# Kernel tuning notes

Hardware: AMD Instinct MI355X
Metric: run time of the kernel (lower is better)

The kernel has to match this reference:

```python
import jax, jax.numpy as jnp
import numpy as np

B, D, L, H, E = 65536, 3, 64, 256, 8
N_HIDDEN_EXTRA = 2  # num_hidden_layers - 1


def setup_inputs() -> dict:
    key = jax.random.key(0)
    ks = jax.random.split(key, 12)
    s = 0.05
    return {
        "x": jax.random.normal(ks[0], (B, D), jnp.float32),
        "labels": jax.random.randint(ks[1], (B,), 0, E, jnp.int64),
        "eps": jax.random.normal(ks[2], (B, L), jnp.float32),
        "mu_table": jax.random.normal(ks[3], (E, L), jnp.float32) * s,
        "logvar_table": jax.random.normal(ks[4], (E, L), jnp.float32) * s,
        "W0": jax.random.normal(ks[5], (E, D + L, H), jnp.float32) * s,
        "b0": jnp.zeros((E, H), jnp.float32),
        "Wh": jax.random.normal(ks[6], (N_HIDDEN_EXTRA, E, H, H), jnp.float32) * s,
        "bh": jnp.zeros((N_HIDDEN_EXTRA, E, H), jnp.float32),
        "Wo": jax.random.normal(ks[7], (E, H, 1), jnp.float32) * s,
        "bo": jnp.zeros((E, 1), jnp.float32),
    }


def reference(x, labels, eps, mu_table, logvar_table, W0, b0, Wh, bh, Wo, bo):
    batch = x.shape[0]
    # encoder: embedding lookup by label
    mu = mu_table[labels]          # [B, L]
    logvar = logvar_table[labels]  # [B, L]
    z = mu + eps * jnp.exp(0.5 * logvar)
    kl = -0.5 * jnp.sum(1.0 + logvar - mu * mu - jnp.exp(logvar)) / batch
    x_in = jnp.concatenate([x, z], axis=1)  # [B, D+L]
    # MoE dispatch: run each expert on the full batch, mask by label
    out = jnp.zeros((batch, 1), x.dtype)
    n_exp = W0.shape[0]
    n_hid = Wh.shape[0]
    for e in range(n_exp):
        h = jax.nn.relu(x_in @ W0[e] + b0[e])
        for l in range(n_hid):
            h = jax.nn.relu(h @ Wh[l, e] + bh[l, e])
        oe = h @ Wo[e] + bo[e]  # [B, 1]
        out = out + jnp.where((labels == e)[:, None], oe, 0.0)
    return out, kl
```

## Files before the change

### kernel.cpp

```cpp
#include <hip/hip_runtime.h>
#include <hip/hip_bf16.h>
#include <stdint.h>

#define B_N 65536
#define L_N 64
#define E_N 8
#define SPB 64
#define MAXT (B_N/SPB + E_N)
#define NHB 256
#define NPW 608
typedef __attribute__((ext_vector_type(4))) float f32x4;
typedef __attribute__((ext_vector_type(8))) short short8;

__device__ __forceinline__ short f2bf(float f){
  union { float f; unsigned u; } v; v.f = f;
  unsigned r = (v.u + 0x7fffu + ((v.u >> 16) & 1u)) >> 16;
  return (short)r;
}

__global__ void k_prep(const int* __restrict__ labels,
                       const float* __restrict__ W0, const float* __restrict__ Wh,
                       unsigned* __restrict__ pcnt,
                       short* __restrict__ wf0, short* __restrict__ wf1){
  const int bid = blockIdx.x, tid = threadIdx.x;
  if(bid < NHB){
    __shared__ unsigned lc[8];
    if(tid < 8) lc[tid] = 0;
    __syncthreads();
    atomicAdd(&lc[labels[bid*256 + tid] & 7], 1u);
    __syncthreads();
    if(tid < 8) pcnt[bid*8 + tid] = lc[tid];
    return;
  }
  int uid = (bid - NHB) * 256 + tid;
  const int NU0 = 8*3*16*64;
  const int NU1 = 2*8*8*16*64;
  if(uid < NU0){
    int e = uid / 3072, r = uid % 3072;
    int s = r / 1024, r2 = r % 1024, t = r2 / 64, l = r2 % 64;
    int g = l >> 4, m = 16*t + (l & 15);
    short8 v;
    #pragma unroll
    for(int j=0;j<8;j++){
      int k = 32*s + 4*g + (j & 3) + 16*(j >> 2);
      float f = (k < 67) ? W0[(e*67 + k)*256 + m] : 0.f;
      v[j] = f2bf(f);
    }
    *(short8*)(wf0 + (size_t)uid * 8) = v;
  } else if(uid < NU0 + NU1){
    int u = uid - NU0;
    int lh = u / 65536, r = u % 65536;
    int e = r / 8192, r1 = r % 8192;
    int s = r1 / 1024, r2 = r1 % 1024, t = r2 / 64, l = r2 % 64;
    int g = l >> 4, m = 16*t + (l & 15);
    short8 v;
    #pragma unroll
    for(int j=0;j<8;j++){
      int k = 32*s + 4*g + (j & 3) + 16*(j >> 2);
      v[j] = f2bf(Wh[(((size_t)(lh*8 + e))*256 + k)*256 + m]);
    }
    *(short8*)(wf1 + (size_t)u * 8) = v;
  }
}

__global__ __launch_bounds__(256) void k_route(
    const int* __restrict__ labels, const unsigned* __restrict__ pcnt,
    int* __restrict__ perm, int* __restrict__ te, int* __restrict__ tb,
    int* __restrict__ tl, const float* __restrict__ mu_t,
    const float* __restrict__ lv_t, float* __restrict__ klout){
  __shared__ unsigned spc[NHB*8];
  __shared__ unsigned ptot[256], ppre[256];
  __shared__ unsigned cnt[8], lbase[8], lcnt[8];
  __shared__ int off[9], ts[9];
  __shared__ float fe[8];
  const int bid = blockIdx.x, tid = threadIdx.x;

  #pragma unroll
  for(int i=0;i<8;i++) spc[tid + i*256] = pcnt[tid + i*256];
  if(tid < 8) lcnt[tid] = 0;
  __syncthreads();

  {
    int e = tid >> 5, c = tid & 31;
    unsigned tot = 0, pre = 0;
    #pragma unroll
    for(int j=0;j<8;j++){
      int b = c*8 + j;
      unsigned v = spc[b*8 + e];
      tot += v;
      if(b < bid) pre += v;
    }
    ptot[tid] = tot; ppre[tid] = pre;
  }
  __syncthreads();
  if(tid < 8){
    unsigned t0 = 0, p0 = 0;
    for(int c=0;c<32;c++){ t0 += ptot[tid*32+c]; p0 += ppre[tid*32+c]; }
    cnt[tid] = t0; ppre[tid] = p0;
  }
  __syncthreads();
  if(tid == 0){
    int o = 0, tt = 0;
    for(int e=0;e<8;e++){ off[e]=o; ts[e]=tt; o += (int)cnt[e]; tt += ((int)cnt[e]+SPB-1)/SPB; }
    off[8]=o; ts[8]=tt;
  }
  __syncthreads();
  if(tid < 8) lbase[tid] = (unsigned)off[tid] + ppre[tid];
  __syncthreads();

  int i = bid*256 + tid;
  int e = labels[i] & 7;
  unsigned r = atomicAdd(&lcnt[e], 1u);
  perm[lbase[e] + r] = i;

  if(bid == 0){
    for(int i2=tid; i2<MAXT; i2+=256){
      if(i2 < ts[8]){
        int ee = 0;
        while(ee < 7 && i2 >= ts[ee+1]) ee++;
        te[i2] = ee; tb[i2] = off[ee] + (i2 - ts[ee])*SPB; tl[i2] = off[ee] + (int)cnt[ee];
      } else { te[i2] = 0; tb[i2] = 0; tl[i2] = 0; }
    }
    if(tid < 8){
      float s = 0.f;
      for(int q=0;q<64;q++){
        float m = mu_t[tid*64+q], l = lv_t[tid*64+q];
        s += 1.f + l - m*m - expf(l);
      }
      fe[tid] = s * (float)cnt[tid];
    }
    __syncthreads();
    if(tid == 0){
      float kl = 0.f;
      for(int e2=0;e2<8;e2++) kl += fe[e2];
      klout[0] = -0.5f * kl / (float)B_N;
    }
  }
}

__global__ __launch_bounds__(256, 3) void k_mlp(
    const float* __restrict__ x, const float* __restrict__ eps,
    const float* __restrict__ mu_t, const float* __restrict__ lv_t,
    const float* __restrict__ b0, const float* __restrict__ bh,
    const float* __restrict__ Wo, const float* __restrict__ bo,
    const short* __restrict__ wf0, const short* __restrict__ wf1,
    const int* __restrict__ perm, const int* __restrict__ te,
    const int* __restrict__ tb, const int* __restrict__ tl,
    float* __restrict__ out)
{
  __shared__ __align__(16) short abuf[3][8192];
  __shared__ __align__(16) float bias_lds[3][256];
  __shared__ __align__(16) float wo_lds[256];

  const int tid  = threadIdx.x;
  const int w    = tid >> 6, lane = tid & 63;
  const int g    = lane >> 4, col = lane & 15;
  const int bid  = blockIdx.x;
  const int e = te[bid], base = tb[bid], lim = tl[bid];
  if(base >= lim) return;

  bias_lds[0][tid] = b0[e*256 + tid];
  bias_lds[1][tid] = bh[e*256 + tid];
  bias_lds[2][tid] = bh[(8 + e)*256 + tid];
  wo_lds[tid]      = Wo[e*256 + tid];

  const int pos = base + w*16 + col;
  const bool valid = pos < lim;
  const int sid = perm[valid ? pos : (lim - 1)];
  const float bo_e = bo[e];

  short8 bx[3];
  #pragma unroll
  for(int s=0;s<3;s++){
    short8 v;
    #pragma unroll
    for(int jh=0;jh<2;jh++){
      #pragma unroll
      for(int q=0;q<4;q++){
        int k = 32*s + 4*g + 16*jh + q;
        float f = 0.f;
        if(k < 3) f = x[sid*3 + k];
        else if(k < 67){
          int zi = k - 3;
          f = mu_t[e*64 + zi] + eps[(size_t)sid*64 + zi] * __expf(0.5f * lv_t[e*64 + zi]);
        }
        v[jh*4 + q] = f2bf(f);
      }
    }
    bx[s] = v;
  }

  const short* w0e = wf0 + (size_t)e * (3*8192);
  const short* w1e = wf1 + (size_t)(0*8 + e) * (8*8192);
  const short* w2e = wf1 + (size_t)(1*8 + e) * (8*8192);

  f32x4 acc[16];
  #pragma unroll
  for(int t=0;t<16;t++) acc[t] = (f32x4){0.f,0.f,0.f,0.f};
  short8 hb[8];

  auto stage = [&](const short* srcT, int bufidx){
    #pragma unroll
    for(int c=0;c<4;c++){
      const char* gp = (const char*)srcT + c*4096 + tid*16;
      char* lp = (char*)&abuf[bufidx][0] + c*4096 + w*1024;
      __builtin_amdgcn_global_load_lds((const __attribute__((address_space(1))) void*)gp,
                                       (__attribute__((address_space(3))) void*)lp, 16, 0, 0);
    }
  };

  auto compute = [&](int bufidx, short8 b){
    const char* ab = (const char*)&abuf[bufidx][0];
    __builtin_amdgcn_s_setprio(1);
    #pragma unroll
    for(int t=0;t<16;t++){
      short8 a = *(const short8*)(ab + t*1024 + lane*16);
      acc[t] = __builtin_amdgcn_mfma_f32_16x16x32_bf16(a, b, acc[t], 0, 0, 0);
    }
    __builtin_amdgcn_s_setprio(0);
  };

  auto epilogue = [&](const float* bias_row){
    #pragma unroll
    for(int t=0;t<16;t++){
      f32x4 b4 = *(const f32x4*)(bias_row + 16*t + 4*g);
      #pragma unroll
      for(int r=0;r<4;r++){
        float vv = acc[t][r] + b4[r];
        acc[t][r] = vv > 0.f ? vv : 0.f;
      }
    }
    #pragma unroll
    for(int s=0;s<8;s++){
      short8 h;
      #pragma unroll
      for(int r=0;r<4;r++){ h[r] = f2bf(acc[2*s][r]); h[4+r] = f2bf(acc[2*s+1][r]); }
      hb[s] = h;
    }
    #pragma unroll
    for(int t=0;t<16;t++) acc[t] = (f32x4){0.f,0.f,0.f,0.f};
  };

  #define SRC_OF(u) ((u) < 3 ? (w0e + (u)*8192) : (u) < 11 ? (w1e + ((u)-3)*8192) \
                             : (w2e + ((u)-11)*8192))
  #define DO_TILE(T, H)                                                           \
    { if((T) < 17){ asm volatile("s_waitcnt vmcnt(4) lgkmcnt(0)" ::: "memory"); } \
      else        { asm volatile("s_waitcnt vmcnt(0) lgkmcnt(0)" ::: "memory"); } \
      __builtin_amdgcn_s_barrier();                                               \
      if((T) + 2 < 19) stage(SRC_OF((T)+2 < 19 ? (T)+2 : 18), ((T)+2) % 3);       \
      compute((T) % 3, H); }

  stage(SRC_OF(0), 0);
  stage(SRC_OF(1), 1);

  DO_TILE(0, bx[0])
  DO_TILE(1, bx[1])
  DO_TILE(2, bx[2])
  epilogue(&bias_lds[0][0]);

  DO_TILE(3,  hb[0])
  DO_TILE(4,  hb[1])
  DO_TILE(5,  hb[2])
  DO_TILE(6,  hb[3])
  DO_TILE(7,  hb[4])
  DO_TILE(8,  hb[5])
  DO_TILE(9,  hb[6])
  DO_TILE(10, hb[7])
  epilogue(&bias_lds[1][0]);

  DO_TILE(11, hb[0])
  DO_TILE(12, hb[1])
  DO_TILE(13, hb[2])
  DO_TILE(14, hb[3])
  DO_TILE(15, hb[4])
  DO_TILE(16, hb[5])
  DO_TILE(17, hb[6])
  DO_TILE(18, hb[7])
  #undef DO_TILE
  #undef SRC_OF

  float dot = 0.f;
  #pragma unroll
  for(int t=0;t<16;t++){
    f32x4 b4 = *(const f32x4*)(&bias_lds[2][16*t + 4*g]);
    f32x4 w4 = *(const f32x4*)(&wo_lds[16*t + 4*g]);
    #pragma unroll
    for(int r=0;r<4;r++){
      float vv = acc[t][r] + b4[r];
      vv = vv > 0.f ? vv : 0.f;
      dot += vv * w4[r];
    }
  }
  dot += __shfl_xor(dot, 16, 64);
  dot += __shfl_xor(dot, 32, 64);
  if(g == 0 && valid) out[sid] = dot + bo_e;
}

extern "C" void kernel_launch(void* const* d_in, const int* in_sizes, int n_in,
                              void* d_out, int out_size, void* d_ws, size_t ws_size,
                              hipStream_t stream){
  (void)in_sizes; (void)n_in; (void)out_size; (void)ws_size;
  const float* x   = (const float*)d_in[0];
  const int*   lab = (const int*)d_in[1];
  const float* eps = (const float*)d_in[2];
  const float* mu  = (const float*)d_in[3];
  const float* lv  = (const float*)d_in[4];
  const float* W0  = (const float*)d_in[5];
  const float* b0  = (const float*)d_in[6];
  const float* Wh  = (const float*)d_in[7];
  const float* bh  = (const float*)d_in[8];
  const float* Wo  = (const float*)d_in[9];
  const float* bo  = (const float*)d_in[10];
  float* out = (float*)d_out;

  char* ws = (char*)d_ws;
  unsigned* pcnt  = (unsigned*)(ws + 128);
  int* te   = (int*)(ws + 16640);
  int* tb   = (int*)(ws + 16640 + 4*MAXT);
  int* tl   = (int*)(ws + 16640 + 8*MAXT);
  int* perm = (int*)(ws + 32768);
  short* wf0 = (short*)(ws + 294912);
  short* wf1 = (short*)(ws + 688128);

  k_prep<<<NHB + NPW, 256, 0, stream>>>(lab, W0, Wh, pcnt, wf0, wf1);
  k_route<<<NHB, 256, 0, stream>>>(lab, pcnt, perm, te, tb, tl, mu, lv, out + B_N);
  k_mlp<<<MAXT, 256, 0, stream>>>(x, eps, mu, lv, b0, bh, Wo, bo,
                                  wf0, wf1, perm, te, tb, tl, out);
}
```

Baseline: 52.76 us.

## Split MLP tile by output columns per wave, share activations via LDS

Each wave now computes a 64-column slice of the hidden output for all 64 samples, instead of all 256 columns for its own 16 samples. Each wave therefore loads only its 4 A-fragments per staged weight tile, and the B-fragments (activations) for all four sample groups are exchanged through a new LDS buffer. Epilogues write bf16 activations to LDS behind added barriers. The final dot product is reduced across waves through LDS. Bias and Wo are read directly from global memory, and launch bounds drop to 2 blocks per SM to accommodate the extra LDS and registers.

```diff
diff --git a/kernel.cpp b/kernel.cpp
--- a/kernel.cpp
+++ b/kernel.cpp
@@ -138,7 +138,7 @@
   }
 }
 
-__global__ __launch_bounds__(256, 3) void k_mlp(
+__global__ __launch_bounds__(256, 2) void k_mlp(
     const float* __restrict__ x, const float* __restrict__ eps,
     const float* __restrict__ mu_t, const float* __restrict__ lv_t,
     const float* __restrict__ b0, const float* __restrict__ bh,
@@ -149,8 +149,7 @@
     float* __restrict__ out)
 {
   __shared__ __align__(16) short abuf[3][8192];
-  __shared__ __align__(16) float bias_lds[3][256];
-  __shared__ __align__(16) float wo_lds[256];
+  __shared__ __align__(16) short bfrag[4][8][64][8];
 
   const int tid  = threadIdx.x;
   const int w    = tid >> 6, lane = tid & 63;
@@ -159,35 +158,30 @@
   const int e = te[bid], base = tb[bid], lim = tl[bid];
   if(base >= lim) return;
 
-  bias_lds[0][tid] = b0[e*256 + tid];
-  bias_lds[1][tid] = bh[e*256 + tid];
-  bias_lds[2][tid] = bh[(8 + e)*256 + tid];
-  wo_lds[tid]      = Wo[e*256 + tid];
-
-  const int pos = base + w*16 + col;
-  const bool valid = pos < lim;
-  const int sid = perm[valid ? pos : (lim - 1)];
   const float bo_e = bo[e];
 
-  short8 bx[3];
-  #pragma unroll
-  for(int s=0;s<3;s++){
-    short8 v;
-    #pragma unroll
-    for(int jh=0;jh<2;jh++){
-      #pragma unroll
-      for(int q=0;q<4;q++){
-        int k = 32*s + 4*g + 16*jh + q;
-        float f = 0.f;
-        if(k < 3) f = x[sid*3 + k];
-        else if(k < 67){
-          int zi = k - 3;
-          f = mu_t[e*64 + zi] + eps[(size_t)sid*64 + zi] * __expf(0.5f * lv_t[e*64 + zi]);
+  {
+    const int pos = base + w*16 + col;
+    const int sid = perm[(pos < lim) ? pos : (lim - 1)];
+    #pragma unroll
+    for(int s=0;s<3;s++){
+      short8 v;
+      #pragma unroll
+      for(int jh=0;jh<2;jh++){
+        #pragma unroll
+        for(int q=0;q<4;q++){
+          int k = 32*s + 4*g + 16*jh + q;
+          float f = 0.f;
+          if(k < 3) f = x[sid*3 + k];
+          else if(k < 67){
+            int zi = k - 3;
+            f = mu_t[e*64 + zi] + eps[(size_t)sid*64 + zi] * __expf(0.5f * lv_t[e*64 + zi]);
+          }
+          v[jh*4 + q] = f2bf(f);
         }
-        v[jh*4 + q] = f2bf(f);
       }
-    }
-    bx[s] = v;
+      *(short8*)&bfrag[w][s][lane][0] = v;
+    }
   }
 
   const short* w0e = wf0 + (size_t)e * (3*8192);
@@ -197,7 +191,6 @@
   f32x4 acc[16];
   #pragma unroll
   for(int t=0;t<16;t++) acc[t] = (f32x4){0.f,0.f,0.f,0.f};
-  short8 hb[8];
 
   auto stage = [&](const short* srcT, int bufidx){
     #pragma unroll
@@ -209,91 +202,130 @@
     }
   };
 
-  auto compute = [&](int bufidx, short8 b){
+  auto compute = [&](int bufidx, int s){
     const char* ab = (const char*)&abuf[bufidx][0];
+    short8 bq[4], aq[4];
+    #pragma unroll
+    for(int q=0;q<4;q++) bq[q] = *(const short8*)&bfrag[q][s][lane][0];
+    #pragma unroll
+    for(int t=0;t<4;t++) aq[t] = *(const short8*)(ab + (w*4 + t)*1024 + lane*16);
     __builtin_amdgcn_s_setprio(1);
     #pragma unroll
-    for(int t=0;t<16;t++){
-      short8 a = *(const short8*)(ab + t*1024 + lane*16);
-      acc[t] = __builtin_amdgcn_mfma_f32_16x16x32_bf16(a, b, acc[t], 0, 0, 0);
-    }
+    for(int t=0;t<4;t++)
+      #pragma unroll
+      for(int q=0;q<4;q++)
+        acc[t*4+q] = __builtin_amdgcn_mfma_f32_16x16x32_bf16(aq[t], bq[q], acc[t*4+q], 0, 0, 0);
     __builtin_amdgcn_s_setprio(0);
   };
 
-  auto epilogue = [&](const float* bias_row){
-    #pragma unroll
-    for(int t=0;t<16;t++){
-      f32x4 b4 = *(const f32x4*)(bias_row + 16*t + 4*g);
-      #pragma unroll
-      for(int r=0;r<4;r++){
-        float vv = acc[t][r] + b4[r];
-        acc[t][r] = vv > 0.f ? vv : 0.f;
+  auto epilogue = [&](const float* bias_g){
+    f32x4 bv[4];
+    #pragma unroll
+    for(int t=0;t<4;t++) bv[t] = *(const f32x4*)(bias_g + 64*w + 16*t + 4*g);
+    #pragma unroll
+    for(int t=0;t<4;t++)
+      #pragma unroll
+      for(int q=0;q<4;q++)
+        #pragma unroll
+        for(int r=0;r<4;r++){
+          float vv = acc[t*4+q][r] + bv[t][r];
+          acc[t*4+q][r] = vv > 0.f ? vv : 0.f;
+        }
+    #pragma unroll
+    for(int u=0;u<2;u++)
+      #pragma unroll
+      for(int q=0;q<4;q++){
+        short8 h;
+        #pragma unroll
+        for(int r=0;r<4;r++){
+          h[r]   = f2bf(acc[(2*u)*4   + q][r]);
+          h[4+r] = f2bf(acc[(2*u+1)*4 + q][r]);
+        }
+        *(short8*)&bfrag[q][2*w+u][lane][0] = h;
       }
-    }
-    #pragma unroll
-    for(int s=0;s<8;s++){
-      short8 h;
-      #pragma unroll
-      for(int r=0;r<4;r++){ h[r] = f2bf(acc[2*s][r]); h[4+r] = f2bf(acc[2*s+1][r]); }
-      hb[s] = h;
-    }
     #pragma unroll
     for(int t=0;t<16;t++) acc[t] = (f32x4){0.f,0.f,0.f,0.f};
   };
 
   #define SRC_OF(u) ((u) < 3 ? (w0e + (u)*8192) : (u) < 11 ? (w1e + ((u)-3)*8192) \
                              : (w2e + ((u)-11)*8192))
-  #define DO_TILE(T, H)                                                           \
+  #define DO_TILE(T, S)                                                           \
     { if((T) < 17){ asm volatile("s_waitcnt vmcnt(4) lgkmcnt(0)" ::: "memory"); } \
       else        { asm volatile("s_waitcnt vmcnt(0) lgkmcnt(0)" ::: "memory"); } \
       __builtin_amdgcn_s_barrier();                                               \
       if((T) + 2 < 19) stage(SRC_OF((T)+2 < 19 ? (T)+2 : 18), ((T)+2) % 3);       \
-      compute((T) % 3, H); }
+      compute((T) % 3, (S)); }
+  #define LAYER_FENCE                                                             \
+    asm volatile("s_waitcnt lgkmcnt(0)" ::: "memory");                            \
+    __builtin_amdgcn_s_barrier();
 
   stage(SRC_OF(0), 0);
   stage(SRC_OF(1), 1);
 
-  DO_TILE(0, bx[0])
-  DO_TILE(1, bx[1])
-  DO_TILE(2, bx[2])
-  epilogue(&bias_lds[0][0]);
-
-  DO_TILE(3,  hb[0])
-  DO_TILE(4,  hb[1])
-  DO_TILE(5,  hb[2])
-  DO_TILE(6,  hb[3])
-  DO_TILE(7,  hb[4])
-  DO_TILE(8,  hb[5])
-  DO_TILE(9,  hb[6])
-  DO_TILE(10, hb[7])
-  epilogue(&bias_lds[1][0]);
-
-  DO_TILE(11, hb[0])
-  DO_TILE(12, hb[1])
-  DO_TILE(13, hb[2])
-  DO_TILE(14, hb[3])
-  DO_TILE(15, hb[4])
-  DO_TILE(16, hb[5])
-  DO_TILE(17, hb[6])
-  DO_TILE(18, hb[7])
+  DO_TILE(0, 0)
+  DO_TILE(1, 1)
+  DO_TILE(2, 2)
+  LAYER_FENCE
+  epilogue(b0 + e*256);
+
+  DO_TILE(3,  0)
+  DO_TILE(4,  1)
+  DO_TILE(5,  2)
+  DO_TILE(6,  3)
+  DO_TILE(7,  4)
+  DO_TILE(8,  5)
+  DO_TILE(9,  6)
+  DO_TILE(10, 7)
+  LAYER_FENCE
+  epilogue(bh + e*256);
+
+  DO_TILE(11, 0)
+  DO_TILE(12, 1)
+  DO_TILE(13, 2)
+  DO_TILE(14, 3)
+  DO_TILE(15, 4)
+  DO_TILE(16, 5)
+  DO_TILE(17, 6)
+  DO_TILE(18, 7)
   #undef DO_TILE
   #undef SRC_OF
 
-  float dot = 0.f;
-  #pragma unroll
-  for(int t=0;t<16;t++){
-    f32x4 b4 = *(const f32x4*)(&bias_lds[2][16*t + 4*g]);
-    f32x4 w4 = *(const f32x4*)(&wo_lds[16*t + 4*g]);
-    #pragma unroll
-    for(int r=0;r<4;r++){
-      float vv = acc[t][r] + b4[r];
-      vv = vv > 0.f ? vv : 0.f;
-      dot += vv * w4[r];
-    }
-  }
-  dot += __shfl_xor(dot, 16, 64);
-  dot += __shfl_xor(dot, 32, 64);
-  if(g == 0 && valid) out[sid] = dot + bo_e;
+  LAYER_FENCE
+  float* odot = (float*)&bfrag[0][0][0][0];
+  {
+    const float* bias_g = bh + (8 + e)*256;
+    const float* wo_g   = Wo + e*256;
+    f32x4 bv[4], wv[4];
+    #pragma unroll
+    for(int t=0;t<4;t++){
+      bv[t] = *(const f32x4*)(bias_g + 64*w + 16*t + 4*g);
+      wv[t] = *(const f32x4*)(wo_g   + 64*w + 16*t + 4*g);
+    }
+    #pragma unroll
+    for(int q=0;q<4;q++){
+      float d = 0.f;
+      #pragma unroll
+      for(int t=0;t<4;t++)
+        #pragma unroll
+        for(int r=0;r<4;r++){
+          float vv = acc[t*4+q][r] + bv[t][r];
+          vv = vv > 0.f ? vv : 0.f;
+          d += vv * wv[t][r];
+        }
+      d += __shfl_xor(d, 16, 64);
+      d += __shfl_xor(d, 32, 64);
+      if(g == 0) odot[(w*4 + q)*16 + col] = d;
+    }
+  }
+  LAYER_FENCE
+  if(tid < 64){
+    int q = tid >> 4, c = tid & 15;
+    float s = odot[(0*4+q)*16+c] + odot[(1*4+q)*16+c]
+            + odot[(2*4+q)*16+c] + odot[(3*4+q)*16+c];
+    int p2 = base + tid;
+    if(p2 < lim) out[perm[p2]] = s + bo_e;
+  }
+  #undef LAYER_FENCE
 }
 
 extern "C" void kernel_launch(void* const* d_in, const int* in_sizes, int n_in,
```

After: 67.02 us. +27.0%, slower.
